# Kernel optimization log

Hardware: AMD Instinct MI355X
Metric: run time of the kernel (lower is better)

Reference implementation:

```python
import jax, jax.numpy as jnp
import numpy as np

B, S, D, H = 32, 512, 768, 12
HD = D // H
FF = 4 * D
EPS = 1e-5


def layernorm(x, g, b):
    mu = jnp.mean(x, axis=-1, keepdims=True)
    var = jnp.mean(jnp.square(x - mu), axis=-1, keepdims=True)
    return (x - mu) * jax.lax.rsqrt(var + EPS) * g + b


def setup_inputs() -> dict:
    key = jax.random.key(0)
    ks = jax.random.split(key, 10)
    s = 0.02
    return {
        "x": jax.random.normal(ks[0], (B, S, D), jnp.float32),
        "edge_bias": jax.random.normal(ks[1], (H, S, S), jnp.float32) * s,
        "ln1_g": jnp.ones((D,), jnp.float32),
        "ln1_b": jnp.zeros((D,), jnp.float32),
        "qkv_w": jax.random.normal(ks[2], (3 * D, D), jnp.float32) * s,
        "qkv_b": jnp.zeros((3 * D,), jnp.float32),
        "proj_w": jax.random.normal(ks[3], (D, D), jnp.float32) * s,
        "proj_b": jnp.zeros((D,), jnp.float32),
        "ln2_g": jnp.ones((D,), jnp.float32),
        "ln2_b": jnp.zeros((D,), jnp.float32),
        "fc1_w": jax.random.normal(ks[4], (FF, D), jnp.float32) * s,
        "fc1_b": jnp.zeros((FF,), jnp.float32),
        "fc2_w": jax.random.normal(ks[5], (D, FF), jnp.float32) * s,
        "fc2_b": jnp.zeros((D,), jnp.float32),
    }


def reference(x, edge_bias, ln1_g, ln1_b, qkv_w, qkv_b, proj_w, proj_b,
              ln2_g, ln2_b, fc1_w, fc1_b, fc2_w, fc2_b):
    shortcut = x
    xn = layernorm(x, ln1_g, ln1_b)
    # qkv: [B,S,3D] -> [3,B,H,S,HD]
    qkv = (xn @ qkv_w.T + qkv_b).reshape(B, S, 3, H, HD).transpose(2, 0, 3, 1, 4)
    q, k, v = qkv[0], qkv[1], qkv[2]
    q = q * (HD ** -0.5)
    attn = jnp.einsum('bhqd,bhkd->bhqk', q, k) + edge_bias[None]
    attn = jax.nn.softmax(attn, axis=-1)
    o = jnp.einsum('bhqk,bhkd->bhqd', attn, v)
    o = o.transpose(0, 2, 1, 3).reshape(B, S, D)
    o = o @ proj_w.T + proj_b
    x = shortcut + o
    h = layernorm(x, ln2_g, ln2_b)
    h = jax.nn.gelu(h @ fc1_w.T + fc1_b, approximate=False)
    h = h @ fc2_w.T + fc2_b
    return x + h
```

## Files before the change

### kernel.cpp

```cpp
#include <hip/hip_runtime.h>

typedef unsigned short u16;
typedef unsigned int u32;
typedef float f32x4 __attribute__((ext_vector_type(4)));
typedef __bf16 bf16x8 __attribute__((ext_vector_type(8)));

__device__ __forceinline__ u16 f2bf(float f) {
  u32 u = __float_as_uint(f);
  u += 0x7fffu + ((u >> 16) & 1u);
  return (u16)(u >> 16);
}

__device__ __forceinline__ float bf2f(u16 v) {
  return __uint_as_float((u32)v << 16);
}

__device__ __forceinline__ void gload16(const u16* g, u16* l) {
  __builtin_amdgcn_global_load_lds(
      (__attribute__((address_space(1))) void*)(u16*)g,
      (__attribute__((address_space(3))) void*)l, 16, 0, 0);
}

__device__ __forceinline__ void packw(const float* __restrict__ in,
                                      u16* __restrict__ o, int N, int K, int i) {
  const int ng = K >> 3;
  const int n = i / ng;
  const int k = (i - n * ng) * 8;
  const float4 f0 = reinterpret_cast<const float4*>(in + (size_t)n * K + k)[0];
  const float4 f1 = reinterpret_cast<const float4*>(in + (size_t)n * K + k)[1];
  u32 p0 = (u32)f2bf(f0.x) | ((u32)f2bf(f0.y) << 16);
  u32 p1 = (u32)f2bf(f0.z) | ((u32)f2bf(f0.w) << 16);
  u32 p2 = (u32)f2bf(f1.x) | ((u32)f2bf(f1.y) << 16);
  u32 p3 = (u32)f2bf(f1.z) | ((u32)f2bf(f1.w) << 16);
  u16* dst = o + ((size_t)(k >> 5) * N + n) * 32 + (k & 31);
  reinterpret_cast<uint4*>(dst)[0] = make_uint4(p0, p1, p2, p3);
}

__global__ __launch_bounds__(256) void cvt_all(
    const float* __restrict__ qkvw, const float* __restrict__ projw,
    const float* __restrict__ fc1w, const float* __restrict__ fc2w,
    const float* __restrict__ ebias, u16* __restrict__ wq, u16* __restrict__ wp,
    u16* __restrict__ wf1, u16* __restrict__ wf2, u16* __restrict__ ebb) {
  int id = blockIdx.x * 256 + threadIdx.x;
  if (id < 786432) {
    float4 f = reinterpret_cast<const float4*>(ebias)[id];
    u32 lo = (u32)f2bf(f.x) | ((u32)f2bf(f.y) << 16);
    u32 hi = (u32)f2bf(f.z) | ((u32)f2bf(f.w) << 16);
    reinterpret_cast<uint2*>(ebb)[id] = make_uint2(lo, hi);
    return;
  }
  id -= 786432;
  if (id < 221184) { packw(qkvw, wq, 2304, 768, id); return; }
  id -= 221184;
  if (id < 73728) { packw(projw, wp, 768, 768, id); return; }
  id -= 73728;
  if (id < 294912) { packw(fc1w, wf1, 3072, 768, id); return; }
  id -= 294912;
  if (id < 294912) packw(fc2w, wf2, 768, 3072, id);
}

__global__ __launch_bounds__(192) void ln_bf16(const float* __restrict__ x,
                                               const float* __restrict__ g,
                                               const float* __restrict__ b,
                                               u16* __restrict__ o) {
  const int row = blockIdx.x;
  const int t = threadIdx.x;
  const float4 a = reinterpret_cast<const float4*>(x + (size_t)row * 768)[t];
  float s = a.x + a.y + a.z + a.w;
  float ss = a.x * a.x + a.y * a.y + a.z * a.z + a.w * a.w;
#pragma unroll
  for (int m = 1; m < 64; m <<= 1) {
    s += __shfl_xor(s, m);
    ss += __shfl_xor(ss, m);
  }
  __shared__ float sb[6];
  if ((t & 63) == 0) { sb[t >> 6] = s; sb[3 + (t >> 6)] = ss; }
  __syncthreads();
  s = sb[0] + sb[1] + sb[2];
  ss = sb[3] + sb[4] + sb[5];
  const float mu = s * (1.0f / 768.0f);
  const float var = ss * (1.0f / 768.0f) - mu * mu;
  const float rs = rsqrtf(var + 1e-5f);
  const int col = t * 4;
  const float4 gv = reinterpret_cast<const float4*>(g)[t];
  const float4 bv = reinterpret_cast<const float4*>(b)[t];
  u32 lo = (u32)f2bf((a.x - mu) * rs * gv.x + bv.x) |
           ((u32)f2bf((a.y - mu) * rs * gv.y + bv.y) << 16);
  u32 hi = (u32)f2bf((a.z - mu) * rs * gv.z + bv.z) |
           ((u32)f2bf((a.w - mu) * rs * gv.w + bv.w) << 16);
  *reinterpret_cast<uint2*>(
      &o[((size_t)(col >> 5) * 16384 + row) * 32 + (col & 31)]) =
      make_uint2(lo, hi);
}

enum { EPI_QKV = 0, EPI_PROJ = 1, EPI_GELU = 2, EPI_OUT = 3 };

__device__ __forceinline__ void read_b4(const u16* sb_, int wn, int lc, int sg,
                                        bf16x8* bf) {
#pragma unroll
  for (int ni = 0; ni < 4; ++ni)
    bf[ni] = *reinterpret_cast<const bf16x8*>(&sb_[(wn * 64 + ni * 16 + lc) * 32 + sg]);
}

__device__ __forceinline__ void read_a01(const u16* sa_, int wm, int lc, int sg,
                                         bf16x8* af) {
#pragma unroll
  for (int mi = 0; mi < 2; ++mi)
    af[mi] = *reinterpret_cast<const bf16x8*>(&sa_[(wm * 128 + mi * 16 + lc) * 32 + sg]);
}

__device__ __forceinline__ void read_a27(const u16* sa_, int wm, int lc, int sg,
                                         bf16x8* af) {
#pragma unroll
  for (int mi = 2; mi < 8; ++mi)
    af[mi] = *reinterpret_cast<const bf16x8*>(&sa_[(wm * 128 + mi * 16 + lc) * 32 + sg]);
}

template <int EPI>
__global__ __launch_bounds__(512, 2) void gemm_bt(
    const u16* __restrict__ A, const u16* __restrict__ W,
    const float* __restrict__ bias, const float* __restrict__ res,
    float* __restrict__ outf, u16* __restrict__ outb,
    u16* __restrict__ outq, u16* __restrict__ outk, u16* __restrict__ outv,
    int M, int N, int K) {
  __shared__ u16 SA[4 * 8192];
  __shared__ u16 SB[4 * 8192];
  const int tid = threadIdx.x;
  const int wid = tid >> 6, l = tid & 63;
  const int wm = wid >> 2, wn = wid & 3;
  const int lg = l >> 4, lc = l & 15;

  const u32 nbn = gridDim.x;
  const u32 orig = blockIdx.y * nbn + blockIdx.x;
  const u32 cpx = (nbn * gridDim.y) >> 3;
  const u32 wgid = (orig & 7) * cpx + (orig >> 3);
  const int bn = wgid % nbn;
  const int bm = wgid / nbn;

  const size_t Msl = (size_t)M * 32;
  const size_t Nsl = (size_t)N * 32;
  const size_t lane_a = (size_t)(bm * 256 + wid * 16 + (l >> 2)) * 32 +
                        (((l & 3) ^ ((l >> 3) & 3)) << 3);
  const size_t lane_w = (size_t)(bn * 256 + wid * 16 + (l >> 2)) * 32 +
                        (((l & 3) ^ ((l >> 3) & 3)) << 3);
  const int sg = (lg ^ ((lc >> 1) & 3)) << 3;

  f32x4 acc[8][4] = {};

  const int NU = K >> 5;

#define STAGE(u)                                                      \
  {                                                                   \
    const u16* Au_ = A + (size_t)(u) * Msl + lane_a;                  \
    const u16* Wu_ = W + (size_t)(u) * Nsl + lane_w;                  \
    gload16(Au_, &SA[((u) & 3) * 8192 + wid * 512]);                  \
    gload16(Au_ + 4096, &SA[((u) & 3) * 8192 + 4096 + wid * 512]);    \
    gload16(Wu_, &SB[((u) & 3) * 8192 + wid * 512]);                  \
    gload16(Wu_ + 4096, &SB[((u) & 3) * 8192 + 4096 + wid * 512]);    \
  }

#define MFMA32(AF, BF)                                                        \
  {                                                                           \
    __builtin_amdgcn_s_setprio(1);                                            \
    _Pragma("unroll") for (int mi = 0; mi < 8; ++mi)                          \
        _Pragma("unroll") for (int ni = 0; ni < 4; ++ni) acc[mi][ni] =        \
            __builtin_amdgcn_mfma_f32_16x16x32_bf16(AF[mi], BF[ni],           \
                                                    acc[mi][ni], 0, 0, 0);    \
    __builtin_amdgcn_s_setprio(0);                                            \
  }

  bf16x8 afA[8], bfA[4], afB[8], bfB[4];

  STAGE(0);
  STAGE(1);
  STAGE(2);
  asm volatile("s_waitcnt vmcnt(4)" ::: "memory");
  __builtin_amdgcn_s_barrier();
  read_b4(&SB[0], wn, lc, sg, bfA);
  read_a01(&SA[0], wm, lc, sg, afA);

  for (int u = 0; u < NU; u += 2) {
    read_a27(&SA[(u & 3) * 8192], wm, lc, sg, afA);
    if (u + 3 < NU) STAGE(u + 3);
    read_b4(&SB[((u + 1) & 3) * 8192], wn, lc, sg, bfB);
    read_a01(&SA[((u + 1) & 3) * 8192], wm, lc, sg, afB);
    MFMA32(afA, bfA);
    if (u + 3 < NU) {
      asm volatile("s_waitcnt vmcnt(4)" ::: "memory");
    } else if (u + 2 < NU) {
      asm volatile("s_waitcnt vmcnt(0)" ::: "memory");
    }
    __builtin_amdgcn_s_barrier();
    read_a27(&SA[((u + 1) & 3) * 8192], wm, lc, sg, afB);
    if (u + 4 < NU) STAGE(u + 4);
    if (u + 2 < NU) {
      read_b4(&SB[((u + 2) & 3) * 8192], wn, lc, sg, bfA);
      read_a01(&SA[((u + 2) & 3) * 8192], wm, lc, sg, afA);
    }
    MFMA32(afB, bfB);
    if (u + 4 < NU) {
      asm volatile("s_waitcnt vmcnt(4)" ::: "memory");
    } else if (u + 3 < NU) {
      asm volatile("s_waitcnt vmcnt(0)" ::: "memory");
    }
    __builtin_amdgcn_s_barrier();
  }
#undef STAGE
#undef MFMA32

  const int rbase = bm * 256 + wm * 128;
  const int cbase = bn * 256 + wn * 64;
#pragma unroll
  for (int mi = 0; mi < 8; ++mi) {
#pragma unroll
    for (int ni = 0; ni < 4; ++ni) {
#pragma unroll
      for (int r = 0; r < 4; ++r) {
        const int i = rbase + mi * 16 + lg * 4 + r;
        const int j = cbase + ni * 16 + lc;
        float v = acc[mi][ni][r] + bias[j];
        if constexpr (EPI == EPI_QKV) {
          const int t = j / 768;
          const int rr = j - t * 768;
          const int h = rr >> 6, hd = rr & 63;
          const int bb = i >> 9, ssi = i & 511;
          if (t == 0) {
            outq[((size_t)(bb * 12 + h) * 512 + ssi) * 64 + hd] = f2bf(v * 0.125f);
          } else if (t == 1) {
            outk[((size_t)(bb * 12 + h) * 512 + ssi) * 64 + hd] = f2bf(v);
          } else {
            outv[((size_t)(bb * 12 + h) * 64 + hd) * 512 + ssi] = f2bf(v);
          }
        } else if constexpr (EPI == EPI_PROJ) {
          outf[(size_t)i * 768 + j] = v + res[(size_t)i * 768 + j];
        } else if constexpr (EPI == EPI_GELU) {
          float z = -1.5957691216f * v - 0.07135481627f * v * v * v;
          float gl = v * __builtin_amdgcn_rcpf(1.0f + __expf(z));
          outb[((size_t)(j >> 5) * 16384 + i) * 32 + (j & 31)] = f2bf(gl);
        } else {
          outf[(size_t)i * 768 + j] = v + res[(size_t)i * 768 + j];
        }
      }
    }
  }
}

__global__ __launch_bounds__(256) void attn_fwd(const u16* __restrict__ q,
                                                const u16* __restrict__ k,
                                                const u16* __restrict__ vt,
                                                const u16* __restrict__ ebb,
                                                u16* __restrict__ o) {
  __shared__ u16 Ks[128 * 64];
  __shared__ u16 Vs[64 * 128];
  __shared__ u16 P[4 * 1024];
  const int tid = threadIdx.x;
  const int w = tid >> 6, l = tid & 63;
  const int lg = l >> 4, lc = l & 15;
  const int xcd = blockIdx.x & 7;
  const int wg = xcd * 384 + (blockIdx.x >> 3);
  const int qt = wg & 7;
  const int b = (wg >> 3) & 31;
  const int h = wg >> 8;
  const int bh = b * 12 + h;
  const int q0 = qt * 64;
  const u16* qp = q + (size_t)bh * 512 * 64;
  const u16* kp = k + (size_t)bh * 512 * 64;
  const u16* vtp = vt + (size_t)bh * 64 * 512;
  const u16* bp = ebb + (size_t)h * 262144 + (size_t)(q0 + w * 16 + lg * 4) * 512 + lc;

  bf16x8 aq[2];
#pragma unroll
  for (int kk = 0; kk < 2; ++kk)
    aq[kk] = *reinterpret_cast<const bf16x8*>(qp + (q0 + w * 16 + lc) * 64 + kk * 32 + lg * 8);

  float m[4], lsum[4];
  f32x4 oa[4] = {};
#pragma unroll
  for (int r = 0; r < 4; ++r) { m[r] = -1e30f; lsum[r] = 0.f; }

  const int krow_l = l >> 3;
  const int kgr = ((l & 7) ^ (l >> 3)) << 3;
  const int vrow_l = l >> 4;
  const int vswz = 4 * (w & 1) + (l >> 4);
  const int vgr = (((l & 15) ^ vswz)) << 3;
  char* Pw = (char*)&P[w * 1024];

  for (int kc = 0; kc < 4; ++kc) {
    const int kb = kc * 128;
    __syncthreads();
#pragma unroll
    for (int i = 0; i < 4; ++i) {
      const int grp = i * 4 + w;
      gload16(kp + (size_t)(kb + grp * 8 + krow_l) * 64 + kgr, &Ks[grp * 512]);
      gload16(vtp + (size_t)(grp * 4 + vrow_l) * 512 + kb + vgr, &Vs[grp * 512]);
    }
    __syncthreads();

    f32x4 s[8] = {};
#pragma unroll
    for (int kt = 0; kt < 8; ++kt) {
      const int kbyte = (kt * 16 + lc) * 128;
      const int sw = lc & 7;
      bf16x8 b0 = *reinterpret_cast<const bf16x8*>((const char*)Ks + kbyte + ((lg ^ sw) << 4));
      bf16x8 b1 = *reinterpret_cast<const bf16x8*>((const char*)Ks + kbyte + (((4 + lg) ^ sw) << 4));
      s[kt] = __builtin_amdgcn_mfma_f32_16x16x32_bf16(aq[0], b0, s[kt], 0, 0, 0);
      s[kt] = __builtin_amdgcn_mfma_f32_16x16x32_bf16(aq[1], b1, s[kt], 0, 0, 0);
    }
#pragma unroll
    for (int kt = 0; kt < 8; ++kt)
#pragma unroll
      for (int r = 0; r < 4; ++r)
        s[kt][r] += bf2f(bp[(size_t)r * 512 + kb + kt * 16]);
#pragma unroll
    for (int r = 0; r < 4; ++r) {
      float mc = s[0][r];
#pragma unroll
      for (int kt = 1; kt < 8; ++kt) mc = fmaxf(mc, s[kt][r]);
      mc = fmaxf(mc, __shfl_xor(mc, 1));
      mc = fmaxf(mc, __shfl_xor(mc, 2));
      mc = fmaxf(mc, __shfl_xor(mc, 4));
      mc = fmaxf(mc, __shfl_xor(mc, 8));
      const float mn = fmaxf(m[r], mc);
      const float al = __expf(m[r] - mn);
      m[r] = mn;
      float sum = 0.f;
#pragma unroll
      for (int kt = 0; kt < 8; ++kt) {
        float pv = __expf(s[kt][r] - mn);
        s[kt][r] = pv;
        sum += pv;
      }
      sum += __shfl_xor(sum, 1);
      sum += __shfl_xor(sum, 2);
      sum += __shfl_xor(sum, 4);
      sum += __shfl_xor(sum, 8);
      lsum[r] = lsum[r] * al + sum;
#pragma unroll
      for (int ni = 0; ni < 4; ++ni) oa[ni][r] *= al;
    }
#pragma unroll
    for (int kt = 0; kt < 8; ++kt)
#pragma unroll
      for (int r = 0; r < 4; ++r) {
        const int row = lg * 4 + r;
        int byte = (row << 8) + ((kt * 16 + lc) << 1);
        byte ^= (row & 7) << 4;
        *reinterpret_cast<u16*>(Pw + byte) = f2bf(s[kt][r]);
      }
#pragma unroll
    for (int ks = 0; ks < 4; ++ks) {
      int pbyte = (lc << 8) + ks * 64 + lg * 16;
      pbyte ^= (lc & 7) << 4;
      bf16x8 pa = *reinterpret_cast<const bf16x8*>(Pw + pbyte);
#pragma unroll
      for (int ni = 0; ni < 4; ++ni) {
        const int vbyte = (ni * 16 + lc) * 256 + (((ks * 4 + lg) ^ (lc & 7)) << 4);
        bf16x8 bv = *reinterpret_cast<const bf16x8*>((const char*)Vs + vbyte);
        oa[ni] = __builtin_amdgcn_mfma_f32_16x16x32_bf16(pa, bv, oa[ni], 0, 0, 0);
      }
    }
  }

  float inv[4];
#pragma unroll
  for (int r = 0; r < 4; ++r) inv[r] = 1.0f / lsum[r];
#pragma unroll
  for (int ni = 0; ni < 4; ++ni)
#pragma unroll
    for (int r = 0; r < 4; ++r) {
      const int i = b * 512 + q0 + w * 16 + lg * 4 + r;
      const int j = h * 64 + ni * 16 + lc;
      o[((size_t)(j >> 5) * 16384 + i) * 32 + (j & 31)] = f2bf(oa[ni][r] * inv[r]);
    }
}

extern "C" void kernel_launch(void* const* d_in, const int* in_sizes, int n_in,
                              void* d_out, int out_size, void* d_ws, size_t ws_size,
                              hipStream_t stream) {
  const float* x     = (const float*)d_in[0];
  const float* ebias = (const float*)d_in[1];
  const float* ln1g  = (const float*)d_in[2];
  const float* ln1b  = (const float*)d_in[3];
  const float* qkvw  = (const float*)d_in[4];
  const float* qkvb  = (const float*)d_in[5];
  const float* projw = (const float*)d_in[6];
  const float* projb = (const float*)d_in[7];
  const float* ln2g  = (const float*)d_in[8];
  const float* ln2b  = (const float*)d_in[9];
  const float* fc1w  = (const float*)d_in[10];
  const float* fc1b  = (const float*)d_in[11];
  const float* fc2w  = (const float*)d_in[12];
  const float* fc2b  = (const float*)d_in[13];
  float* out = (float*)d_out;

  char* p = (char*)d_ws;
  const size_t ACT = (size_t)16384 * 768 * 2;
  u16* xnb = (u16*)(p);
  u16* qb  = (u16*)(p + ACT);
  u16* kb  = (u16*)(p + 2 * ACT);
  u16* vb  = (u16*)(p + 3 * ACT);
  u16* ffb = (u16*)(p + 4 * ACT);
  u16* ebb = (u16*)(p + 4 * ACT);
  float* x2 = (float*)(p + 4 * ACT + (size_t)16384 * 3072 * 2);
  char* wz = p + 4 * ACT + (size_t)16384 * 3072 * 2 + (size_t)16384 * 768 * 4;
  u16* wq  = (u16*)wz;
  u16* wp  = wq + (size_t)2304 * 768;
  u16* wf1 = wp + (size_t)768 * 768;
  u16* wf2 = wf1 + (size_t)3072 * 768;

  cvt_all<<<6528, 256, 0, stream>>>(qkvw, projw, fc1w, fc2w, ebias,
                                    wq, wp, wf1, wf2, ebb);

  ln_bf16<<<16384, 192, 0, stream>>>(x, ln1g, ln1b, xnb);

  gemm_bt<EPI_QKV><<<dim3(9, 64), 512, 0, stream>>>(
      xnb, wq, qkvb, nullptr, nullptr, nullptr, qb, kb, vb, 16384, 2304, 768);

  attn_fwd<<<3072, 256, 0, stream>>>(qb, kb, vb, ebb, xnb);

  gemm_bt<EPI_PROJ><<<dim3(3, 64), 512, 0, stream>>>(
      xnb, wp, projb, x, x2, nullptr, nullptr, nullptr, nullptr, 16384, 768, 768);

  ln_bf16<<<16384, 192, 0, stream>>>(x2, ln2g, ln2b, kb);

  gemm_bt<EPI_GELU><<<dim3(12, 64), 512, 0, stream>>>(
      kb, wf1, fc1b, nullptr, nullptr, ffb, nullptr, nullptr, nullptr, 16384, 3072, 768);

  gemm_bt<EPI_OUT><<<dim3(3, 64), 512, 0, stream>>>(
      ffb, wf2, fc2b, x2, out, nullptr, nullptr, nullptr, nullptr, 16384, 768, 3072);
}
```

Before: 500.1 us.

## Restructure GEMM main loop into double-buffered 64-K tiles with quarter-step barriers

Replaces the 4-stage ring of 32-wide K slices with a 2-buffer scheme over 64-wide K tiles. Each tile is split into four MFMA quarters, each preceded by LDS reads, a partial global-to-LDS prefetch, a barrier and an lgkmcnt(0) wait. This interleaves loads and MFMAs more finely and uses fewer A-fragment registers, but adds many barriers per tile and reduces prefetch depth from three slices ahead to one tile ahead.

```diff
diff --git a/kernel.cpp b/kernel.cpp
--- a/kernel.cpp
+++ b/kernel.cpp
@@ -95,27 +95,6 @@
 
 enum { EPI_QKV = 0, EPI_PROJ = 1, EPI_GELU = 2, EPI_OUT = 3 };
 
-__device__ __forceinline__ void read_b4(const u16* sb_, int wn, int lc, int sg,
-                                        bf16x8* bf) {
-#pragma unroll
-  for (int ni = 0; ni < 4; ++ni)
-    bf[ni] = *reinterpret_cast<const bf16x8*>(&sb_[(wn * 64 + ni * 16 + lc) * 32 + sg]);
-}
-
-__device__ __forceinline__ void read_a01(const u16* sa_, int wm, int lc, int sg,
-                                         bf16x8* af) {
-#pragma unroll
-  for (int mi = 0; mi < 2; ++mi)
-    af[mi] = *reinterpret_cast<const bf16x8*>(&sa_[(wm * 128 + mi * 16 + lc) * 32 + sg]);
-}
-
-__device__ __forceinline__ void read_a27(const u16* sa_, int wm, int lc, int sg,
-                                         bf16x8* af) {
-#pragma unroll
-  for (int mi = 2; mi < 8; ++mi)
-    af[mi] = *reinterpret_cast<const bf16x8*>(&sa_[(wm * 128 + mi * 16 + lc) * 32 + sg]);
-}
-
 template <int EPI>
 __global__ __launch_bounds__(512, 2) void gemm_bt(
     const u16* __restrict__ A, const u16* __restrict__ W,
@@ -123,8 +102,8 @@
     float* __restrict__ outf, u16* __restrict__ outb,
     u16* __restrict__ outq, u16* __restrict__ outk, u16* __restrict__ outv,
     int M, int N, int K) {
-  __shared__ u16 SA[4 * 8192];
-  __shared__ u16 SB[4 * 8192];
+  __shared__ u16 SA[2 * 16384];
+  __shared__ u16 SB[2 * 16384];
   const int tid = threadIdx.x;
   const int wid = tid >> 6, l = tid & 63;
   const int wm = wid >> 2, wn = wid & 3;
@@ -147,66 +126,98 @@
 
   f32x4 acc[8][4] = {};
 
-  const int NU = K >> 5;
-
-#define STAGE(u)                                                      \
-  {                                                                   \
-    const u16* Au_ = A + (size_t)(u) * Msl + lane_a;                  \
-    const u16* Wu_ = W + (size_t)(u) * Nsl + lane_w;                  \
-    gload16(Au_, &SA[((u) & 3) * 8192 + wid * 512]);                  \
-    gload16(Au_ + 4096, &SA[((u) & 3) * 8192 + 4096 + wid * 512]);    \
-    gload16(Wu_, &SB[((u) & 3) * 8192 + wid * 512]);                  \
-    gload16(Wu_ + 4096, &SB[((u) & 3) * 8192 + 4096 + wid * 512]);    \
-  }
-
-#define MFMA32(AF, BF)                                                        \
-  {                                                                           \
-    __builtin_amdgcn_s_setprio(1);                                            \
-    _Pragma("unroll") for (int mi = 0; mi < 8; ++mi)                          \
-        _Pragma("unroll") for (int ni = 0; ni < 4; ++ni) acc[mi][ni] =        \
-            __builtin_amdgcn_mfma_f32_16x16x32_bf16(AF[mi], BF[ni],           \
-                                                    acc[mi][ni], 0, 0, 0);    \
-    __builtin_amdgcn_s_setprio(0);                                            \
-  }
-
-  bf16x8 afA[8], bfA[4], afB[8], bfB[4];
-
-  STAGE(0);
-  STAGE(1);
-  STAGE(2);
-  asm volatile("s_waitcnt vmcnt(4)" ::: "memory");
-  __builtin_amdgcn_s_barrier();
-  read_b4(&SB[0], wn, lc, sg, bfA);
-  read_a01(&SA[0], wm, lc, sg, afA);
-
-  for (int u = 0; u < NU; u += 2) {
-    read_a27(&SA[(u & 3) * 8192], wm, lc, sg, afA);
-    if (u + 3 < NU) STAGE(u + 3);
-    read_b4(&SB[((u + 1) & 3) * 8192], wn, lc, sg, bfB);
-    read_a01(&SA[((u + 1) & 3) * 8192], wm, lc, sg, afB);
-    MFMA32(afA, bfA);
-    if (u + 3 < NU) {
+  const int NT = K >> 6;
+
+#define STAGE_A(T1, s, n)                                               \
+  {                                                                     \
+    const u16* Au_ = A + (size_t)(2 * (T1) + (s)) * Msl + lane_a;       \
+    gload16(Au_, &SA[(n) * 16384 + (s) * 8192 + wid * 512]);            \
+    gload16(Au_ + 4096, &SA[(n) * 16384 + (s) * 8192 + 4096 + wid * 512]); \
+  }
+#define STAGE_B(T1, s, n)                                               \
+  {                                                                     \
+    const u16* Wu_ = W + (size_t)(2 * (T1) + (s)) * Nsl + lane_w;       \
+    gload16(Wu_, &SB[(n) * 16384 + (s) * 8192 + wid * 512]);            \
+    gload16(Wu_ + 4096, &SB[(n) * 16384 + (s) * 8192 + 4096 + wid * 512]); \
+  }
+#define RDA(c, ks, mh)                                                  \
+  {                                                                     \
+    _Pragma("unroll") for (int mi = 0; mi < 4; ++mi) afq[mi] =          \
+        *reinterpret_cast<const bf16x8*>(                               \
+            &SA[(c) * 16384 + (ks) * 8192 +                             \
+                (wm * 128 + ((mh) * 4 + mi) * 16 + lc) * 32 + sg]);     \
+  }
+#define RDB(c, ks, dst)                                                 \
+  {                                                                     \
+    _Pragma("unroll") for (int ni = 0; ni < 4; ++ni) dst[ni] =          \
+        *reinterpret_cast<const bf16x8*>(                               \
+            &SB[(c) * 16384 + (ks) * 8192 +                             \
+                (wn * 64 + ni * 16 + lc) * 32 + sg]);                   \
+  }
+#define MM(mh, BK)                                                      \
+  {                                                                     \
+    __builtin_amdgcn_s_setprio(1);                                      \
+    _Pragma("unroll") for (int mi = 0; mi < 4; ++mi)                    \
+        _Pragma("unroll") for (int ni = 0; ni < 4; ++ni)                \
+            acc[(mh) * 4 + mi][ni] =                                    \
+                __builtin_amdgcn_mfma_f32_16x16x32_bf16(                \
+                    afq[mi], BK[ni], acc[(mh) * 4 + mi][ni], 0, 0, 0);  \
+    __builtin_amdgcn_s_setprio(0);                                      \
+  }
+#define LGKM0 asm volatile("s_waitcnt lgkmcnt(0)" ::: "memory")
+#define BAR __builtin_amdgcn_s_barrier()
+
+  STAGE_A(0, 0, 0);
+  STAGE_A(0, 1, 0);
+  STAGE_B(0, 0, 0);
+  STAGE_B(0, 1, 0);
+  asm volatile("s_waitcnt vmcnt(0)" ::: "memory");
+  BAR;
+
+  for (int T = 0; T < NT; ++T) {
+    const int c = T & 1, n = c ^ 1;
+    const bool st = (T + 1 < NT);
+    bf16x8 afq[4], bk0[4], bk1[4];
+    RDA(c, 0, 0);
+    RDB(c, 0, bk0);
+    if (st) STAGE_A(T + 1, 0, n);
+    BAR;
+    LGKM0;
+    MM(0, bk0);
+    BAR;
+    RDA(c, 0, 1);
+    if (st) STAGE_B(T + 1, 0, n);
+    BAR;
+    LGKM0;
+    MM(1, bk0);
+    if (st) {
       asm volatile("s_waitcnt vmcnt(4)" ::: "memory");
-    } else if (u + 2 < NU) {
+    } else {
       asm volatile("s_waitcnt vmcnt(0)" ::: "memory");
     }
-    __builtin_amdgcn_s_barrier();
-    read_a27(&SA[((u + 1) & 3) * 8192], wm, lc, sg, afB);
-    if (u + 4 < NU) STAGE(u + 4);
-    if (u + 2 < NU) {
-      read_b4(&SB[((u + 2) & 3) * 8192], wn, lc, sg, bfA);
-      read_a01(&SA[((u + 2) & 3) * 8192], wm, lc, sg, afA);
-    }
-    MFMA32(afB, bfB);
-    if (u + 4 < NU) {
-      asm volatile("s_waitcnt vmcnt(4)" ::: "memory");
-    } else if (u + 3 < NU) {
-      asm volatile("s_waitcnt vmcnt(0)" ::: "memory");
-    }
-    __builtin_amdgcn_s_barrier();
-  }
-#undef STAGE
-#undef MFMA32
+    BAR;
+    RDA(c, 1, 0);
+    RDB(c, 1, bk1);
+    if (st) STAGE_A(T + 1, 1, n);
+    BAR;
+    LGKM0;
+    MM(0, bk1);
+    BAR;
+    RDA(c, 1, 1);
+    if (st) STAGE_B(T + 1, 1, n);
+    BAR;
+    LGKM0;
+    MM(1, bk1);
+    if (st) asm volatile("s_waitcnt vmcnt(4)" ::: "memory");
+    BAR;
+  }
+#undef STAGE_A
+#undef STAGE_B
+#undef RDA
+#undef RDB
+#undef MM
+#undef LGKM0
+#undef BAR
 
   const int rbase = bm * 256 + wm * 128;
   const int cbase = bn * 256 + wn * 64;
```

Result: no change. 499.4 us (median of 3 runs) (-0.1%).

## Load GEMM A operand directly from global into registers, bypassing LDS

Applied to the files above, without the earlier changes.

The GEMM no longer stages the A tile in shared memory. Each wave now reads its A fragments straight from global memory into registers every K step, while B keeps its 4-stage LDS pipeline. The loop drops the two-step register double buffering and runs one MFMA block per iteration. This frees half the LDS and removes the A LDS writes and reads. In exchange, global latency is exposed right before the MFMAs, and the four waves sharing a row block read the same A data redundantly. The vmcnt(2) wait also blocks on older B prefetches, which shortens the effective pipeline.

```diff
diff --git a/kernel.cpp b/kernel.cpp
--- a/kernel.cpp
+++ b/kernel.cpp
@@ -95,27 +95,6 @@
 
 enum { EPI_QKV = 0, EPI_PROJ = 1, EPI_GELU = 2, EPI_OUT = 3 };
 
-__device__ __forceinline__ void read_b4(const u16* sb_, int wn, int lc, int sg,
-                                        bf16x8* bf) {
-#pragma unroll
-  for (int ni = 0; ni < 4; ++ni)
-    bf[ni] = *reinterpret_cast<const bf16x8*>(&sb_[(wn * 64 + ni * 16 + lc) * 32 + sg]);
-}
-
-__device__ __forceinline__ void read_a01(const u16* sa_, int wm, int lc, int sg,
-                                         bf16x8* af) {
-#pragma unroll
-  for (int mi = 0; mi < 2; ++mi)
-    af[mi] = *reinterpret_cast<const bf16x8*>(&sa_[(wm * 128 + mi * 16 + lc) * 32 + sg]);
-}
-
-__device__ __forceinline__ void read_a27(const u16* sa_, int wm, int lc, int sg,
-                                         bf16x8* af) {
-#pragma unroll
-  for (int mi = 2; mi < 8; ++mi)
-    af[mi] = *reinterpret_cast<const bf16x8*>(&sa_[(wm * 128 + mi * 16 + lc) * 32 + sg]);
-}
-
 template <int EPI>
 __global__ __launch_bounds__(512, 2) void gemm_bt(
     const u16* __restrict__ A, const u16* __restrict__ W,
@@ -123,7 +102,6 @@
     float* __restrict__ outf, u16* __restrict__ outb,
     u16* __restrict__ outq, u16* __restrict__ outk, u16* __restrict__ outv,
     int M, int N, int K) {
-  __shared__ u16 SA[4 * 8192];
   __shared__ u16 SB[4 * 8192];
   const int tid = threadIdx.x;
   const int wid = tid >> 6, l = tid & 63;
@@ -139,8 +117,7 @@
 
   const size_t Msl = (size_t)M * 32;
   const size_t Nsl = (size_t)N * 32;
-  const size_t lane_a = (size_t)(bm * 256 + wid * 16 + (l >> 2)) * 32 +
-                        (((l & 3) ^ ((l >> 3) & 3)) << 3);
+  const u16* Albase = A + (size_t)(bm * 256 + wm * 128 + lc) * 32 + lg * 8;
   const size_t lane_w = (size_t)(bn * 256 + wid * 16 + (l >> 2)) * 32 +
                         (((l & 3) ^ ((l >> 3) & 3)) << 3);
   const int sg = (lg ^ ((lc >> 1) & 3)) << 3;
@@ -149,64 +126,41 @@
 
   const int NU = K >> 5;
 
-#define STAGE(u)                                                      \
+#define STAGE_B(u)                                                    \
   {                                                                   \
-    const u16* Au_ = A + (size_t)(u) * Msl + lane_a;                  \
     const u16* Wu_ = W + (size_t)(u) * Nsl + lane_w;                  \
-    gload16(Au_, &SA[((u) & 3) * 8192 + wid * 512]);                  \
-    gload16(Au_ + 4096, &SA[((u) & 3) * 8192 + 4096 + wid * 512]);    \
     gload16(Wu_, &SB[((u) & 3) * 8192 + wid * 512]);                  \
     gload16(Wu_ + 4096, &SB[((u) & 3) * 8192 + 4096 + wid * 512]);    \
   }
 
-#define MFMA32(AF, BF)                                                        \
-  {                                                                           \
-    __builtin_amdgcn_s_setprio(1);                                            \
-    _Pragma("unroll") for (int mi = 0; mi < 8; ++mi)                          \
-        _Pragma("unroll") for (int ni = 0; ni < 4; ++ni) acc[mi][ni] =        \
-            __builtin_amdgcn_mfma_f32_16x16x32_bf16(AF[mi], BF[ni],           \
-                                                    acc[mi][ni], 0, 0, 0);    \
-    __builtin_amdgcn_s_setprio(0);                                            \
-  }
-
-  bf16x8 afA[8], bfA[4], afB[8], bfB[4];
-
-  STAGE(0);
-  STAGE(1);
-  STAGE(2);
+  STAGE_B(0);
+  STAGE_B(1);
+  STAGE_B(2);
   asm volatile("s_waitcnt vmcnt(4)" ::: "memory");
   __builtin_amdgcn_s_barrier();
-  read_b4(&SB[0], wn, lc, sg, bfA);
-  read_a01(&SA[0], wm, lc, sg, afA);
-
-  for (int u = 0; u < NU; u += 2) {
-    read_a27(&SA[(u & 3) * 8192], wm, lc, sg, afA);
-    if (u + 3 < NU) STAGE(u + 3);
-    read_b4(&SB[((u + 1) & 3) * 8192], wn, lc, sg, bfB);
-    read_a01(&SA[((u + 1) & 3) * 8192], wm, lc, sg, afB);
-    MFMA32(afA, bfA);
-    if (u + 3 < NU) {
-      asm volatile("s_waitcnt vmcnt(4)" ::: "memory");
-    } else if (u + 2 < NU) {
-      asm volatile("s_waitcnt vmcnt(0)" ::: "memory");
-    }
+
+  for (int u = 0; u < NU; ++u) {
+    bf16x8 af[8], bf[4];
+    const u16* Au = Albase + (size_t)u * Msl;
+#pragma unroll
+    for (int mi = 0; mi < 8; ++mi)
+      af[mi] = *reinterpret_cast<const bf16x8*>(Au + mi * 512);
+    if (u + 3 < NU) STAGE_B(u + 3);
+    const u16* sb_ = &SB[(u & 3) * 8192];
+#pragma unroll
+    for (int ni = 0; ni < 4; ++ni)
+      bf[ni] = *reinterpret_cast<const bf16x8*>(&sb_[(wn * 64 + ni * 16 + lc) * 32 + sg]);
+    asm volatile("s_waitcnt vmcnt(2)" ::: "memory");
+    __builtin_amdgcn_s_setprio(1);
+#pragma unroll
+    for (int mi = 0; mi < 8; ++mi)
+#pragma unroll
+      for (int ni = 0; ni < 4; ++ni)
+        acc[mi][ni] = __builtin_amdgcn_mfma_f32_16x16x32_bf16(af[mi], bf[ni], acc[mi][ni], 0, 0, 0);
+    __builtin_amdgcn_s_setprio(0);
     __builtin_amdgcn_s_barrier();
-    read_a27(&SA[((u + 1) & 3) * 8192], wm, lc, sg, afB);
-    if (u + 4 < NU) STAGE(u + 4);
-    if (u + 2 < NU) {
-      read_b4(&SB[((u + 2) & 3) * 8192], wn, lc, sg, bfA);
-      read_a01(&SA[((u + 2) & 3) * 8192], wm, lc, sg, afA);
-    }
-    MFMA32(afB, bfB);
-    if (u + 4 < NU) {
-      asm volatile("s_waitcnt vmcnt(4)" ::: "memory");
-    } else if (u + 3 < NU) {
-      asm volatile("s_waitcnt vmcnt(0)" ::: "memory");
-    }
-    __builtin_amdgcn_s_barrier();
-  }
-#undef STAGE
-#undef MFMA32
+  }
+#undef STAGE_B
 
   const int rbase = bm * 256 + wm * 128;
   const int cbase = bn * 256 + wn * 64;
```

New measurement: 682.7 us. 1.37x slower.
